# Optimization experiments

Measured on AMD Instinct MI355X. Metric: run time of the kernel, lower is better.

Reference implementation:

```python
import math
import jax, jax.numpy as jnp
import numpy as np

NUM_HEADS = 16
HEAD_DIM = 128
BLOCK = 256
EPS = 1e-6


def _get_slopes(n):
    def p2(n):
        start = 2 ** (-2 ** (-(math.log2(n) - 3)))
        return [start * start ** i for i in range(n)]
    if math.log2(n).is_integer():
        return p2(n)
    c = 2 ** math.floor(math.log2(n))
    return p2(c) + _get_slopes(2 * c)[0::2][: n - c]


def setup_inputs() -> dict:
    key = jax.random.key(0)
    ks = jax.random.split(key, 4)
    d_in, d_out = 2048, 2048
    x = jax.random.normal(ks[0], (2, 4096, d_in), dtype=jnp.float32)
    Wqkv = jax.random.normal(ks[1], (d_in, 3 * NUM_HEADS * HEAD_DIM), dtype=jnp.float32) * 0.02
    Wg = jax.random.normal(ks[2], (d_in, NUM_HEADS * HEAD_DIM), dtype=jnp.float32) * 0.02
    Wout = jax.random.normal(ks[3], (NUM_HEADS * HEAD_DIM, d_out), dtype=jnp.float32) * 0.02
    norm_w = jnp.ones((NUM_HEADS * HEAD_DIM,), dtype=jnp.float32)
    return {"x": x, "Wqkv": Wqkv, "Wg": Wg, "Wout": Wout, "norm_w": norm_w}


def reference(x, Wqkv, Wg, Wout, norm_w):
    b, n, _ = x.shape
    h, d = NUM_HEADS, HEAD_DIM
    nb = n // BLOCK  # seq_len chosen divisible by block_size

    # slopes (ALiBi-style), shape [h,1,1]
    slope = jnp.asarray(_get_slopes(h), dtype=jnp.float32).reshape(h, 1, 1)

    qkv = jax.nn.silu(x @ Wqkv)                       # [b,n,3hd]
    qkv = qkv.reshape(b, n, h, 3 * d)
    q, k, v = jnp.split(qkv, 3, axis=-1)              # each [b,n,h,d]
    q = q.transpose(0, 2, 1, 3)                       # [b,h,n,d]
    k = k.transpose(0, 2, 1, 3)
    v = v.transpose(0, 2, 1, 3)

    # per-position decay factors within a block
    arr = jnp.arange(BLOCK, dtype=jnp.float32) + 1.0          # [B]
    q_decay = jnp.exp(-slope * arr[:, None])                  # [h,B,1]
    k_decay = jnp.exp(-slope * (BLOCK - arr[:, None]))        # [h,B,1]
    idx = arr[:, None] - arr[None, :]                         # [B,B]
    diag_decay = jnp.where(idx >= 0, jnp.exp(-slope[None] * idx[None, None]), 0.0)  # [1,h,B,B]
    block_decay = jnp.exp(-slope * BLOCK)                     # [h,1,1]

    # blocked xs: [nb, b, h, B, d]
    def to_blocks(t):
        return t.reshape(b, h, nb, BLOCK, d).transpose(2, 0, 1, 3, 4)

    qb, kb, vb = to_blocks(q), to_blocks(k), to_blocks(v)

    def step(kv, blk):
        qi, ki, vi = blk                                       # [b,h,B,d]
        # inter-block: (qi * q_decay) @ kv  -> [b,h,B,d]
        non_diag = jnp.einsum('bhmd,bhde->bhme', qi * q_decay, kv)
        # intra-block causal decayed attention
        qk = jnp.einsum('bhmd,bhnd->bhmn', qi, ki) * diag_decay
        diag = jnp.einsum('bhmn,bhne->bhme', qk, vi)
        out = non_diag + diag
        kv_new = block_decay * kv + jnp.einsum('bhmd,bhme->bhde', ki * k_decay, vi)
        return kv_new, out

    kv0 = jnp.zeros((b, h, d, d), dtype=jnp.float32)
    _, out_blocks = jax.lax.scan(step, kv0, (qb, kb, vb))      # [nb,b,h,B,d]
    o = out_blocks.transpose(1, 2, 0, 3, 4).reshape(b, h, n, d)
    o = o.transpose(0, 2, 1, 3).reshape(b, n, h * d)           # [b,n,hd]

    # T5 (RMS) LayerNorm
    var = jnp.mean(o * o, axis=-1, keepdims=True)
    o = o * jax.lax.rsqrt(var + EPS) * norm_w

    # output gate and projection
    o = jax.nn.sigmoid(x @ Wg) * o
    return o @ Wout
```

## Files before the change

### kernel.cpp

```cpp
#include <hip/hip_runtime.h>
#include <cstddef>

typedef float f32x4 __attribute__((ext_vector_type(4)));
typedef __bf16 bf16x8 __attribute__((ext_vector_type(8)));
typedef unsigned short u16x8 __attribute__((ext_vector_type(8)));
typedef unsigned short u16x4 __attribute__((ext_vector_type(4)));

constexpr int NB = 2, S = 4096, H = 16, D = 128;
constexpr int DIN = 2048, NQKV = 6144, HD = 2048;
constexpr int BLK = 256, NBL = 16;

constexpr size_t SZ_XB    = (size_t)NB * S * DIN * 2;
constexpr size_t SZ_WQKVT = (size_t)NQKV * DIN * 2;
constexpr size_t SZ_WGT   = (size_t)HD * DIN * 2;
constexpr size_t SZ_WOUTT = (size_t)HD * HD * 2;
constexpr size_t SZ_QKVB  = (size_t)NB * S * NQKV * 2;
constexpr size_t SZ_GB    = (size_t)NB * S * HD * 2;
constexpr size_t SZ_ST    = (size_t)NB * H * NBL * D * D * 2;
constexpr size_t SZ_OB    = (size_t)NB * S * HD * 2;

__device__ __forceinline__ float bf2f(unsigned short u) {
  return __uint_as_float(((unsigned)u) << 16);
}
__device__ __forceinline__ unsigned short f2bf(float f) {
  unsigned u = __float_as_uint(f);
  u += 0x7fffu + ((u >> 16) & 1u);
  return (unsigned short)(u >> 16);
}
__device__ __forceinline__ void gload16(const void* g, void* l) {
  __builtin_amdgcn_global_load_lds(
      (const __attribute__((address_space(1))) unsigned int*)g,
      (__attribute__((address_space(3))) unsigned int*)l, 16, 0, 0);
}

__global__ __launch_bounds__(256) void cvt_bf16(
    const float* __restrict__ in, unsigned short* __restrict__ out) {
  const size_t id = (size_t)blockIdx.x * 256 + threadIdx.x;
  const float4 a = *(const float4*)&in[id * 8];
  const float4 c = *(const float4*)&in[id * 8 + 4];
  u16x8 o;
  o[0] = f2bf(a.x); o[1] = f2bf(a.y); o[2] = f2bf(a.z); o[3] = f2bf(a.w);
  o[4] = f2bf(c.x); o[5] = f2bf(c.y); o[6] = f2bf(c.z); o[7] = f2bf(c.w);
  *(u16x8*)&out[id * 8] = o;
}

__global__ __launch_bounds__(256) void transpose_cvt(
    const float* __restrict__ W, unsigned short* __restrict__ Wt, int K, int N) {
  __shared__ unsigned short tile[32][33];
  const int n0 = blockIdx.x * 32, k0 = blockIdx.y * 32;
  const int t = threadIdx.x;
  const int r = t >> 3, c4 = (t & 7) * 4;
  const float4 v = *(const float4*)&W[(size_t)(k0 + r) * N + n0 + c4];
  tile[r][c4 + 0] = f2bf(v.x);
  tile[r][c4 + 1] = f2bf(v.y);
  tile[r][c4 + 2] = f2bf(v.z);
  tile[r][c4 + 3] = f2bf(v.w);
  __syncthreads();
  u16x4 o;
  #pragma unroll
  for (int i = 0; i < 4; ++i) o[i] = tile[c4 + i][r];
  *(u16x4*)&Wt[(size_t)(n0 + r) * K + k0 + c4] = o;
}

template<int ACT>
__global__ __launch_bounds__(512, 2) void gemm256(
    const unsigned short* __restrict__ A, const unsigned short* __restrict__ Bt,
    void* __restrict__ C, int M, int N, int K) {
  __shared__ unsigned short lds[65536];
  char* ldsb = (char*)lds;
  const int t = threadIdx.x;
  const int lane = t & 63, wave = t >> 6;
  const int wr = wave >> 2, wc = wave & 3;

  const int nbm = M >> 8, nbn = N >> 8;
  const int nbmx = nbm >> 3;
  const int xcd = blockIdx.x & 7, q = blockIdx.x >> 3;
  const int bm = xcd * nbmx + (q % nbmx);
  const int bn = q / nbmx;

  const int lrow = lane >> 2;
  const int lcg  = (lane & 3) ^ (lrow & 3);
  const unsigned short* sA0 = A  + (size_t)(bm * 256 + wave * 32 + lrow) * K + lcg * 8;
  const unsigned short* sA1 = A  + (size_t)(bm * 256 + wave * 32 + 16 + lrow) * K + lcg * 8;
  const unsigned short* sB0 = Bt + (size_t)(bn * 256 + wave * 32 + lrow) * K + lcg * 8;
  const unsigned short* sB1 = Bt + (size_t)(bn * 256 + wave * 32 + 16 + lrow) * K + lcg * 8;
  const int dA0 = wave * 2048, dA1 = wave * 2048 + 1024;
  const int dB0 = 16384 + dA0, dB1 = 16384 + dA1;

  const int cgb = (lane >> 4) << 4;
  int offA[8], offB[4];
  #pragma unroll
  for (int m = 0; m < 8; ++m) {
    const int row = wr * 128 + m * 16 + (lane & 15);
    offA[m] = row * 64 + (cgb ^ ((row & 3) << 4));
  }
  #pragma unroll
  for (int n = 0; n < 4; ++n) {
    const int row = wc * 64 + n * 16 + (lane & 15);
    offB[n] = 16384 + row * 64 + (cgb ^ ((row & 3) << 4));
  }

  const int NT = K >> 5;
  #define STG_A(u) { const int _s = ((u) & 3) * 32768; const int _o = (u) * 32; \
    gload16(sA0 + _o, ldsb + _s + dA0); gload16(sA1 + _o, ldsb + _s + dA1); }
  #define STG_B(u) { const int _s = ((u) & 3) * 32768; const int _o = (u) * 32; \
    gload16(sB0 + _o, ldsb + _s + dB0); gload16(sB1 + _o, ldsb + _s + dB1); }

  STG_A(0); STG_B(0); STG_A(1); STG_B(1); STG_A(2); STG_B(2);
  asm volatile("s_waitcnt vmcnt(8)" ::: "memory");
  __builtin_amdgcn_s_barrier();

  f32x4 acc[8][4] = {};
  for (int u = 0; u < NT; ++u) {
    const int slot = (u & 3) * 32768;
    bf16x8 af[4], bf[4];
    #pragma unroll
    for (int n = 0; n < 4; ++n) bf[n] = *(const bf16x8*)(ldsb + slot + offB[n]);
    #pragma unroll
    for (int m = 0; m < 4; ++m) af[m] = *(const bf16x8*)(ldsb + slot + offA[m]);
    if (u + 3 < NT) STG_A(u + 3);
    __builtin_amdgcn_s_barrier();
    __builtin_amdgcn_s_setprio(1);
    #pragma unroll
    for (int m = 0; m < 4; ++m)
      #pragma unroll
      for (int n = 0; n < 4; ++n)
        acc[m][n] = __builtin_amdgcn_mfma_f32_16x16x32_bf16(af[m], bf[n], acc[m][n], 0, 0, 0);
    __builtin_amdgcn_s_setprio(0);
    __builtin_amdgcn_s_barrier();
    #pragma unroll
    for (int m = 0; m < 4; ++m) af[m] = *(const bf16x8*)(ldsb + slot + offA[4 + m]);
    if (u + 3 < NT) STG_B(u + 3);
    if (u < NT - 3)       asm volatile("s_waitcnt vmcnt(8)" ::: "memory");
    else if (u == NT - 3) asm volatile("s_waitcnt vmcnt(4)" ::: "memory");
    else                  asm volatile("s_waitcnt vmcnt(0)" ::: "memory");
    __builtin_amdgcn_s_barrier();
    __builtin_amdgcn_s_setprio(1);
    #pragma unroll
    for (int m = 0; m < 4; ++m)
      #pragma unroll
      for (int n = 0; n < 4; ++n)
        acc[4 + m][n] = __builtin_amdgcn_mfma_f32_16x16x32_bf16(af[m], bf[n], acc[4 + m][n], 0, 0, 0);
    __builtin_amdgcn_s_setprio(0);
    __builtin_amdgcn_s_barrier();
  }
  #undef STG_A
  #undef STG_B

  const int ro = (lane >> 4) * 4, co = lane & 15;
  #pragma unroll
  for (int m = 0; m < 8; ++m)
    #pragma unroll
    for (int n = 0; n < 4; ++n) {
      const int gc = bn * 256 + wc * 64 + n * 16 + co;
      #pragma unroll
      for (int r = 0; r < 4; ++r) {
        const int gr = bm * 256 + wr * 128 + m * 16 + ro + r;
        float v = acc[m][n][r];
        if constexpr (ACT == 1) v = v / (1.f + __expf(-v));
        if constexpr (ACT == 2) v = 1.f / (1.f + __expf(-v));
        if constexpr (ACT == 0) ((float*)C)[(size_t)gr * N + gc] = v;
        else ((unsigned short*)C)[(size_t)gr * N + gc] = f2bf(v);
      }
    }
}

__global__ __launch_bounds__(256) void kv_outer(
    const unsigned short* __restrict__ qkv, unsigned short* __restrict__ st) {
  const int gid = blockIdx.x;
  const int j = gid & 15;
  const int bh = gid >> 4;
  const int h = bh & 15;
  const int b = bh >> 4;
  const float slope = exp2f(-0.5f * (float)(h + 1));
  const int t = threadIdx.x;
  __shared__ unsigned short kl[64][136];
  __shared__ unsigned short vl[64][136];
  float acc[8][8] = {};
  const int e0 = (t >> 4) * 8, f0 = (t & 15) * 8;
  for (int ch = 0; ch < 4; ++ch) {
    if (ch) __syncthreads();
    #pragma unroll
    for (int i = 0; i < 4; ++i) {
      const int cc = t + 256 * i;
      const int r = cc >> 4, c0 = (cc & 15) * 8;
      const int mb = ch * 64 + r;
      const int seq = b * S + j * BLK + mb;
      const u16x8 k8 = *(const u16x8*)&qkv[(size_t)seq * NQKV + h * 384 + 128 + c0];
      const float kd = expf(-slope * (float)(255 - mb));
      u16x8 kw;
      #pragma unroll
      for (int q2 = 0; q2 < 8; ++q2) kw[q2] = f2bf(bf2f(k8[q2]) * kd);
      *(u16x8*)&kl[r][c0] = kw;
      *(u16x8*)&vl[r][c0] = *(const u16x8*)&qkv[(size_t)seq * NQKV + h * 384 + 256 + c0];
    }
    __syncthreads();
    for (int m = 0; m < 64; ++m) {
      const u16x8 k8 = *(const u16x8*)&kl[m][e0];
      const u16x8 v8 = *(const u16x8*)&vl[m][f0];
      float kf[8], vf[8];
      #pragma unroll
      for (int q2 = 0; q2 < 8; ++q2) { kf[q2] = bf2f(k8[q2]); vf[q2] = bf2f(v8[q2]); }
      #pragma unroll
      for (int i = 0; i < 8; ++i)
        #pragma unroll
        for (int q2 = 0; q2 < 8; ++q2) acc[i][q2] += kf[i] * vf[q2];
    }
  }
  const size_t base = (size_t)gid * (D * D);
  #pragma unroll
  for (int q2 = 0; q2 < 8; ++q2) {
    u16x8 ow;
    #pragma unroll
    for (int i = 0; i < 8; ++i) ow[i] = f2bf(acc[i][q2]);
    *(u16x8*)&st[base + (size_t)(f0 + q2) * D + e0] = ow;
  }
}

__global__ __launch_bounds__(256) void kv_scan(unsigned short* __restrict__ st) {
  const int id = blockIdx.x * 256 + threadIdx.x;
  const int ef = id & (D * D - 1);
  const int bh = id >> 14;
  const int h = bh & 15;
  const float slope = exp2f(-0.5f * (float)(h + 1));
  const float bd = expf(-slope * 256.f);
  unsigned short* p = st + (size_t)bh * NBL * D * D + ef;
  float cur = 0.f;
  #pragma unroll
  for (int jj = 0; jj < NBL; ++jj) {
    const float m = bf2f(p[(size_t)jj * D * D]);
    p[(size_t)jj * D * D] = f2bf(cur);
    cur = bd * cur + m;
  }
}

__global__ __launch_bounds__(256) void attn_mfma(
    const unsigned short* __restrict__ qkv, const unsigned short* __restrict__ st,
    unsigned short* __restrict__ ob) {
  const int gid = blockIdx.x;
  const int half = gid & 1;
  const int rest = gid >> 1;
  const int j = rest & 15;
  const int bh = rest >> 4;
  const int h = bh & 15;
  const int b = bh >> 4;
  const float slope = exp2f(-0.5f * (float)(h + 1));
  const int t = threadIdx.x;
  const int lane = t & 63, wave = t >> 6, wr = wave >> 1, wc = wave & 1;

  __shared__ unsigned short ql[128][136];
  __shared__ unsigned short cb[128][136];
  __shared__ unsigned short pl[128][136];

  {
    const int r = t >> 4, c0 = (t & 15) * 8;
    const size_t stbase = (size_t)rest * (D * D);
    #pragma unroll
    for (int p = 0; p < 8; ++p) {
      const int seq = b * S + j * BLK + half * 128 + r + p * 16;
      *(u16x8*)&ql[r + p * 16][c0] = *(const u16x8*)&qkv[(size_t)seq * NQKV + h * 384 + c0];
      *(u16x8*)&cb[r + p * 16][c0] = *(const u16x8*)&st[stbase + (size_t)(r + p * 16) * D + c0];
    }
  }
  __syncthreads();

  f32x4 acc[4][4] = {};
  #pragma unroll
  for (int kk = 0; kk < 4; ++kk) {
    bf16x8 af[4], bfr[4];
    #pragma unroll
    for (int m = 0; m < 4; ++m)
      af[m] = *(const bf16x8*)&ql[wr * 64 + m * 16 + (lane & 15)][kk * 32 + (lane >> 4) * 8];
    #pragma unroll
    for (int n = 0; n < 4; ++n)
      bfr[n] = *(const bf16x8*)&cb[wc * 64 + n * 16 + (lane & 15)][kk * 32 + (lane >> 4) * 8];
    #pragma unroll
    for (int m = 0; m < 4; ++m)
      #pragma unroll
      for (int n = 0; n < 4; ++n)
        acc[m][n] = __builtin_amdgcn_mfma_f32_16x16x32_bf16(af[m], bfr[n], acc[m][n], 0, 0, 0);
  }
  const int ro = (lane >> 4) * 4;
  #pragma unroll
  for (int m = 0; m < 4; ++m)
    #pragma unroll
    for (int r = 0; r < 4; ++r) {
      const int gm = half * 128 + wr * 64 + m * 16 + ro + r;
      const float qd = expf(-slope * (float)(gm + 1));
      #pragma unroll
      for (int n = 0; n < 4; ++n) acc[m][n][r] *= qd;
    }

  const int nch = 1 + half;
  for (int c = 0; c < nch; ++c) {
    __syncthreads();
    {
      const int r = t >> 4, c0 = (t & 15) * 8;
      #pragma unroll
      for (int p = 0; p < 8; ++p) {
        const int seq = b * S + j * BLK + c * 128 + r + p * 16;
        *(u16x8*)&cb[r + p * 16][c0] = *(const u16x8*)&qkv[(size_t)seq * NQKV + h * 384 + 128 + c0];
      }
    }
    __syncthreads();
    f32x4 sacc[4][4] = {};
    #pragma unroll
    for (int kk = 0; kk < 4; ++kk) {
      bf16x8 af[4], bfr[4];
      #pragma unroll
      for (int m = 0; m < 4; ++m)
        af[m] = *(const bf16x8*)&ql[wr * 64 + m * 16 + (lane & 15)][kk * 32 + (lane >> 4) * 8];
      #pragma unroll
      for (int n = 0; n < 4; ++n)
        bfr[n] = *(const bf16x8*)&cb[wc * 64 + n * 16 + (lane & 15)][kk * 32 + (lane >> 4) * 8];
      #pragma unroll
      for (int m = 0; m < 4; ++m)
        #pragma unroll
        for (int n = 0; n < 4; ++n)
          sacc[m][n] = __builtin_amdgcn_mfma_f32_16x16x32_bf16(af[m], bfr[n], sacc[m][n], 0, 0, 0);
    }
    #pragma unroll
    for (int m = 0; m < 4; ++m)
      #pragma unroll
      for (int n = 0; n < 4; ++n) {
        const int lc = wc * 64 + n * 16 + (lane & 15);
        const int gp = c * 128 + lc;
        #pragma unroll
        for (int r = 0; r < 4; ++r) {
          const int lm = wr * 64 + m * 16 + ro + r;
          const int gm = half * 128 + lm;
          const float dd = (gm >= gp) ? expf(-slope * (float)(gm - gp)) : 0.f;
          pl[lm][lc] = f2bf(sacc[m][n][r] * dd);
        }
      }
    __syncthreads();
    {
      const int vr = t & 15, vc0 = (t >> 4) * 8;
      #pragma unroll
      for (int p = 0; p < 8; ++p) {
        const int row = vr + p * 16;
        const int seq = b * S + j * BLK + c * 128 + row;
        const u16x8 vv = *(const u16x8*)&qkv[(size_t)seq * NQKV + h * 384 + 256 + vc0];
        #pragma unroll
        for (int i = 0; i < 8; ++i) cb[vc0 + i][row] = vv[i];
      }
    }
    __syncthreads();
    #pragma unroll
    for (int kk = 0; kk < 4; ++kk) {
      bf16x8 af[4], bfr[4];
      #pragma unroll
      for (int m = 0; m < 4; ++m)
        af[m] = *(const bf16x8*)&pl[wr * 64 + m * 16 + (lane & 15)][kk * 32 + (lane >> 4) * 8];
      #pragma unroll
      for (int n = 0; n < 4; ++n)
        bfr[n] = *(const bf16x8*)&cb[wc * 64 + n * 16 + (lane & 15)][kk * 32 + (lane >> 4) * 8];
      #pragma unroll
      for (int m = 0; m < 4; ++m)
        #pragma unroll
        for (int n = 0; n < 4; ++n)
          acc[m][n] = __builtin_amdgcn_mfma_f32_16x16x32_bf16(af[m], bfr[n], acc[m][n], 0, 0, 0);
    }
  }

  #pragma unroll
  for (int m = 0; m < 4; ++m)
    #pragma unroll
    for (int n = 0; n < 4; ++n) {
      const int fc = h * D + wc * 64 + n * 16 + (lane & 15);
      #pragma unroll
      for (int r = 0; r < 4; ++r) {
        const int seq = b * S + j * BLK + half * 128 + wr * 64 + m * 16 + ro + r;
        ob[(size_t)seq * HD + fc] = f2bf(acc[m][n][r]);
      }
    }
}

__global__ __launch_bounds__(256) void norm_gate(
    const unsigned short* __restrict__ ob, const unsigned short* __restrict__ gb,
    const float* __restrict__ nw, unsigned short* __restrict__ og) {
  const int row = blockIdx.x;
  const int t = threadIdx.x;
  const u16x8 ov = *(const u16x8*)&ob[(size_t)row * HD + t * 8];
  float f[8];
  float ss = 0.f;
  #pragma unroll
  for (int i = 0; i < 8; ++i) { f[i] = bf2f(ov[i]); ss += f[i] * f[i]; }
  #pragma unroll
  for (int off = 32; off > 0; off >>= 1) ss += __shfl_down(ss, off, 64);
  __shared__ float red[4];
  if ((t & 63) == 0) red[t >> 6] = ss;
  __syncthreads();
  const float rms = rsqrtf((red[0] + red[1] + red[2] + red[3]) * (1.f / HD) + 1e-6f);
  const u16x8 gv = *(const u16x8*)&gb[(size_t)row * HD + t * 8];
  u16x8 ow;
  #pragma unroll
  for (int i = 0; i < 8; ++i)
    ow[i] = f2bf(f[i] * rms * nw[t * 8 + i] * bf2f(gv[i]));
  *(u16x8*)&og[(size_t)row * HD + t * 8] = ow;
}

extern "C" void kernel_launch(void* const* d_in, const int* in_sizes, int n_in,
                              void* d_out, int out_size, void* d_ws, size_t ws_size,
                              hipStream_t stream) {
  (void)in_sizes; (void)n_in; (void)out_size; (void)ws_size;
  const float* x    = (const float*)d_in[0];
  const float* Wqkv = (const float*)d_in[1];
  const float* Wg   = (const float*)d_in[2];
  const float* Wout = (const float*)d_in[3];
  const float* nw   = (const float*)d_in[4];

  char* ws = (char*)d_ws;
  unsigned short* xb    = (unsigned short*)ws; ws += SZ_XB;
  unsigned short* wqkvt = (unsigned short*)ws; ws += SZ_WQKVT;
  unsigned short* wgt   = (unsigned short*)ws; ws += SZ_WGT;
  unsigned short* woutt = (unsigned short*)ws; ws += SZ_WOUTT;
  unsigned short* qkvb  = (unsigned short*)ws; ws += SZ_QKVB;
  unsigned short* gb    = (unsigned short*)ws; ws += SZ_GB;
  unsigned short* st    = (unsigned short*)ws; ws += SZ_ST;
  unsigned short* ob    = (unsigned short*)ws; ws += SZ_OB;
  unsigned short* og    = xb;

  cvt_bf16<<<dim3((NB * S * DIN) / (256 * 8)), 256, 0, stream>>>(x, xb);
  transpose_cvt<<<dim3(NQKV / 32, DIN / 32), 256, 0, stream>>>(Wqkv, wqkvt, DIN, NQKV);
  transpose_cvt<<<dim3(HD / 32, DIN / 32), 256, 0, stream>>>(Wg, wgt, DIN, HD);
  transpose_cvt<<<dim3(HD / 32, HD / 32), 256, 0, stream>>>(Wout, woutt, HD, HD);

  gemm256<1><<<dim3((NB * S / 256) * (NQKV / 256)), 512, 0, stream>>>(xb, wqkvt, qkvb, NB * S, NQKV, DIN);
  gemm256<2><<<dim3((NB * S / 256) * (HD / 256)), 512, 0, stream>>>(xb, wgt, gb, NB * S, HD, DIN);

  kv_outer<<<dim3(NB * H * NBL), 256, 0, stream>>>(qkvb, st);
  kv_scan<<<dim3((NB * H * D * D) / 256), 256, 0, stream>>>(st);
  attn_mfma<<<dim3(NB * H * NBL * 2), 256, 0, stream>>>(qkvb, st, ob);

  norm_gate<<<dim3(NB * S), 256, 0, stream>>>(ob, gb, nw, og);
  gemm256<0><<<dim3((NB * S / 256) * (HD / 256)), 512, 0, stream>>>(og, woutt, d_out, NB * S, HD, HD);
}
```

Baseline: 546.8 us.

## Restructure GEMM main loop to K=64 double-buffered tiles with four MFMA phases

The 256x256 bf16 GEMM mainloop now uses K-steps of 64 instead of 32, with two 64 KB LDS buffers replacing four 32 KB slots. It uses a new XOR swizzle over 8 column groups and splits each iteration into four MFMA quadrants, interleaving B-half and A loads with compute. The intent is to halve loop and barrier overhead per unit of K and overlap global loads with MFMA work more evenly. In exchange it adds more LDS-read register pressure and explicit lgkmcnt waits before each compute phase, and the prefetch depth drops from three stages to two.

```diff
diff --git a/kernel.cpp b/kernel.cpp
--- a/kernel.cpp
+++ b/kernel.cpp
@@ -71,6 +71,7 @@
   const int t = threadIdx.x;
   const int lane = t & 63, wave = t >> 6;
   const int wr = wave >> 2, wc = wave & 3;
+  const int l15 = lane & 15;
 
   const int nbm = M >> 8, nbn = N >> 8;
   const int nbmx = nbm >> 3;
@@ -78,74 +79,113 @@
   const int bm = xcd * nbmx + (q % nbmx);
   const int bn = q / nbmx;
 
-  const int lrow = lane >> 2;
-  const int lcg  = (lane & 3) ^ (lrow & 3);
-  const unsigned short* sA0 = A  + (size_t)(bm * 256 + wave * 32 + lrow) * K + lcg * 8;
-  const unsigned short* sA1 = A  + (size_t)(bm * 256 + wave * 32 + 16 + lrow) * K + lcg * 8;
-  const unsigned short* sB0 = Bt + (size_t)(bn * 256 + wave * 32 + lrow) * K + lcg * 8;
-  const unsigned short* sB1 = Bt + (size_t)(bn * 256 + wave * 32 + 16 + lrow) * K + lcg * 8;
-  const int dA0 = wave * 2048, dA1 = wave * 2048 + 1024;
-  const int dB0 = 16384 + dA0, dB1 = 16384 + dA1;
-
-  const int cgb = (lane >> 4) << 4;
-  int offA[8], offB[4];
-  #pragma unroll
-  for (int m = 0; m < 8; ++m) {
-    const int row = wr * 128 + m * 16 + (lane & 15);
-    offA[m] = row * 64 + (cgb ^ ((row & 3) << 4));
-  }
-  #pragma unroll
-  for (int n = 0; n < 4; ++n) {
-    const int row = wc * 64 + n * 16 + (lane & 15);
-    offB[n] = 16384 + row * 64 + (cgb ^ ((row & 3) << 4));
-  }
-
-  const int NT = K >> 5;
-  #define STG_A(u) { const int _s = ((u) & 3) * 32768; const int _o = (u) * 32; \
-    gload16(sA0 + _o, ldsb + _s + dA0); gload16(sA1 + _o, ldsb + _s + dA1); }
-  #define STG_B(u) { const int _s = ((u) & 3) * 32768; const int _o = (u) * 32; \
-    gload16(sB0 + _o, ldsb + _s + dB0); gload16(sB1 + _o, ldsb + _s + dB1); }
-
-  STG_A(0); STG_B(0); STG_A(1); STG_B(1); STG_A(2); STG_B(2);
-  asm volatile("s_waitcnt vmcnt(8)" ::: "memory");
+  const int cg = (t & 7) ^ ((t >> 3) & 7);
+  const unsigned short* sA = A  + (size_t)(bm * 256 + (t >> 3)) * K + cg * 8;
+  const unsigned short* sB = Bt + (size_t)(bn * 256 + (t >> 3)) * K + cg * 8;
+
+  const int s0 = (((lane >> 4) ^ (lane & 7)) << 4);
+  const int s1 = (((4 + (lane >> 4)) ^ (lane & 7)) << 4);
+  const int rB0 = (wc & 1) * 64 + l15;
+  const int hbB = 32768 + (wc >> 1) * 16384;
+  const int haA = wr * 16384;
+
+  #define STG(bufi, isB, h, uu) {                                          \
+    char* _d = ldsb + ((bufi) << 16) + ((isB) ? 32768 : 0) + (h) * 16384 + (t << 4); \
+    const unsigned short* _s = ((isB) ? sB : sA) + (size_t)((h) * 128) * K + (size_t)(uu) * 64; \
+    gload16(_s, _d); gload16(_s + (size_t)64 * K, _d + 8192); }
+
+  const int NT = K >> 6;
+  STG(0, 0, 0, 0); STG(0, 0, 1, 0); STG(0, 1, 0, 0); STG(0, 1, 1, 0);
+  STG(1, 0, 0, 1); STG(1, 0, 1, 1);
+  asm volatile("s_waitcnt vmcnt(4)" ::: "memory");
   __builtin_amdgcn_s_barrier();
 
   f32x4 acc[8][4] = {};
   for (int u = 0; u < NT; ++u) {
-    const int slot = (u & 3) * 32768;
-    bf16x8 af[4], bf[4];
-    #pragma unroll
-    for (int n = 0; n < 4; ++n) bf[n] = *(const bf16x8*)(ldsb + slot + offB[n]);
-    #pragma unroll
-    for (int m = 0; m < 4; ++m) af[m] = *(const bf16x8*)(ldsb + slot + offA[m]);
-    if (u + 3 < NT) STG_A(u + 3);
-    __builtin_amdgcn_s_barrier();
+    const int base = (u & 1) << 16;
+    const int nb = ((u + 1) & 1);
+    bf16x8 af[4][2], bf0[2][2], bf1[2][2];
+    #pragma unroll
+    for (int m = 0; m < 4; ++m) {
+      const int rb = base + haA + (m * 16 + l15) * 128;
+      af[m][0] = *(const bf16x8*)(ldsb + rb + s0);
+      af[m][1] = *(const bf16x8*)(ldsb + rb + s1);
+    }
+    #pragma unroll
+    for (int n = 0; n < 2; ++n) {
+      const int rb = base + hbB + (rB0 + n * 16) * 128;
+      bf0[n][0] = *(const bf16x8*)(ldsb + rb + s0);
+      bf0[n][1] = *(const bf16x8*)(ldsb + rb + s1);
+    }
+    if (u + 1 < NT) STG(nb, 1, 0, u + 1);
+    __builtin_amdgcn_s_barrier();
+    asm volatile("s_waitcnt lgkmcnt(0)" ::: "memory");
+    __builtin_amdgcn_sched_barrier(0);
     __builtin_amdgcn_s_setprio(1);
     #pragma unroll
     for (int m = 0; m < 4; ++m)
       #pragma unroll
-      for (int n = 0; n < 4; ++n)
-        acc[m][n] = __builtin_amdgcn_mfma_f32_16x16x32_bf16(af[m], bf[n], acc[m][n], 0, 0, 0);
+      for (int n = 0; n < 2; ++n)
+        #pragma unroll
+        for (int kk = 0; kk < 2; ++kk)
+          acc[m][n] = __builtin_amdgcn_mfma_f32_16x16x32_bf16(af[m][kk], bf0[n][kk], acc[m][n], 0, 0, 0);
     __builtin_amdgcn_s_setprio(0);
     __builtin_amdgcn_s_barrier();
     #pragma unroll
-    for (int m = 0; m < 4; ++m) af[m] = *(const bf16x8*)(ldsb + slot + offA[4 + m]);
-    if (u + 3 < NT) STG_B(u + 3);
-    if (u < NT - 3)       asm volatile("s_waitcnt vmcnt(8)" ::: "memory");
-    else if (u == NT - 3) asm volatile("s_waitcnt vmcnt(4)" ::: "memory");
-    else                  asm volatile("s_waitcnt vmcnt(0)" ::: "memory");
-    __builtin_amdgcn_s_barrier();
+    for (int n = 0; n < 2; ++n) {
+      const int rb = base + hbB + (rB0 + (2 + n) * 16) * 128;
+      bf1[n][0] = *(const bf16x8*)(ldsb + rb + s0);
+      bf1[n][1] = *(const bf16x8*)(ldsb + rb + s1);
+    }
+    if (u + 1 < NT) STG(nb, 1, 1, u + 1);
+    __builtin_amdgcn_s_barrier();
+    asm volatile("s_waitcnt lgkmcnt(0)" ::: "memory");
+    __builtin_amdgcn_sched_barrier(0);
     __builtin_amdgcn_s_setprio(1);
     #pragma unroll
     for (int m = 0; m < 4; ++m)
       #pragma unroll
-      for (int n = 0; n < 4; ++n)
-        acc[4 + m][n] = __builtin_amdgcn_mfma_f32_16x16x32_bf16(af[m], bf[n], acc[4 + m][n], 0, 0, 0);
+      for (int n = 0; n < 2; ++n)
+        #pragma unroll
+        for (int kk = 0; kk < 2; ++kk)
+          acc[m][2 + n] = __builtin_amdgcn_mfma_f32_16x16x32_bf16(af[m][kk], bf1[n][kk], acc[m][2 + n], 0, 0, 0);
     __builtin_amdgcn_s_setprio(0);
     __builtin_amdgcn_s_barrier();
-  }
-  #undef STG_A
-  #undef STG_B
+    #pragma unroll
+    for (int m = 0; m < 4; ++m) {
+      const int rb = base + haA + ((4 + m) * 16 + l15) * 128;
+      af[m][0] = *(const bf16x8*)(ldsb + rb + s0);
+      af[m][1] = *(const bf16x8*)(ldsb + rb + s1);
+    }
+    __builtin_amdgcn_s_barrier();
+    asm volatile("s_waitcnt lgkmcnt(0)" ::: "memory");
+    __builtin_amdgcn_sched_barrier(0);
+    __builtin_amdgcn_s_setprio(1);
+    #pragma unroll
+    for (int m = 0; m < 4; ++m)
+      #pragma unroll
+      for (int n = 0; n < 2; ++n)
+        #pragma unroll
+        for (int kk = 0; kk < 2; ++kk)
+          acc[4 + m][n] = __builtin_amdgcn_mfma_f32_16x16x32_bf16(af[m][kk], bf0[n][kk], acc[4 + m][n], 0, 0, 0);
+    __builtin_amdgcn_s_setprio(0);
+    __builtin_amdgcn_s_barrier();
+    if (u + 2 < NT) { STG((u & 1), 0, 0, u + 2); STG((u & 1), 0, 1, u + 2); }
+    if (u < NT - 2) asm volatile("s_waitcnt vmcnt(4)" ::: "memory");
+    else            asm volatile("s_waitcnt vmcnt(0)" ::: "memory");
+    __builtin_amdgcn_s_barrier();
+    __builtin_amdgcn_s_setprio(1);
+    #pragma unroll
+    for (int m = 0; m < 4; ++m)
+      #pragma unroll
+      for (int n = 0; n < 2; ++n)
+        #pragma unroll
+        for (int kk = 0; kk < 2; ++kk)
+          acc[4 + m][2 + n] = __builtin_amdgcn_mfma_f32_16x16x32_bf16(af[m][kk], bf1[n][kk], acc[4 + m][2 + n], 0, 0, 0);
+    __builtin_amdgcn_s_setprio(0);
+    __builtin_amdgcn_s_barrier();
+  }
+  #undef STG
 
   const int ro = (lane >> 4) * 4, co = lane & 15;
   #pragma unroll
```

Result: faster. 531.1 us (-2.9%).
